# Kernel optimization log

Measured on AMD Instinct MI355X. Metric: run time of the kernel, lower is better.

## Reference

```python
import jax, jax.numpy as jnp
import numpy as np
from jax import lax

DIM = 1024
BATCH = 16
WIDTH = 2048
DECAY = 0.99


def setup_inputs() -> dict:
    key = jax.random.key(0)
    k1, k2, k3, k4 = jax.random.split(key, 4)
    scale = 1.0 / np.sqrt(DIM)
    x = jax.random.normal(k1, (BATCH, WIDTH, DIM), dtype=jnp.float32)
    state = jnp.zeros((BATCH, DIM), dtype=jnp.float32)
    Wv = jax.random.normal(k2, (DIM, DIM), dtype=jnp.float32) * scale
    Wr = jax.random.normal(k3, (DIM, DIM), dtype=jnp.float32) * scale
    Wc = jax.random.normal(k4, (DIM, DIM), dtype=jnp.float32) * scale
    return {"x": x, "state": state, "Wv": Wv, "Wr": Wr, "Wc": Wc}


def reference(x, state, Wv, Wr, Wc):
    # x: [B, W, D], state: [B, D]; fixed-decay RWKV recurrence along width.
    decay = jnp.asarray(DECAY, dtype=x.dtype)
    one_minus = jnp.asarray(1.0, dtype=x.dtype) - decay
    v = jnp.einsum('bwd,de->bwe', x, Wv)                 # value projection
    r = jax.nn.sigmoid(jnp.einsum('bwd,de->bwe', x, Wr))  # receptance

    # scan over width (time) axis: elems shaped [W, B, D]
    def step(s_prev, inp):
        v_t, r_t, x_t = inp
        s_curr = decay * s_prev + one_minus * v_t
        y_t = x_t + r_t * s_curr
        return s_curr, y_t

    elems = (jnp.swapaxes(v, 0, 1), jnp.swapaxes(r, 0, 1), jnp.swapaxes(x, 0, 1))
    new_state, y_t = lax.scan(step, state, elems)
    y = jnp.swapaxes(y_t, 0, 1)                          # [B, W, D]
    y = y + jnp.einsum('bwd,de->bwe', y, Wc)             # minimal channel mix
    return y, new_state
```

## Files before the change

kernel.cpp:

```cpp
#include <hip/hip_runtime.h>
#include <hip/hip_bf16.h>
#include <math.h>


#define DIMK 1024
#define MROWS 32768
#define NCHUNK 16
#define CHUNKL 128
#define DECAY_F 0.99f
#define OM_F 0.01f

typedef __attribute__((ext_vector_type(8))) short short8;
typedef __attribute__((ext_vector_type(4))) float floatx4;

using bf16 = __hip_bfloat16;
using bf162 = __hip_bfloat162;

__global__ void prep_weights(const float* __restrict__ Wv,
                             const float* __restrict__ Wr,
                             const float* __restrict__ Wc,
                             bf16* __restrict__ WT) {
  __shared__ float tile[32][33];
  const int bk = blockIdx.x * 32;
  const int bn = blockIdx.y * 32;
  const float* src;
  int nbase = bn;
  if (bn < 1024)      { src = Wv; }
  else if (bn < 2048) { src = Wr; nbase = bn - 1024; }
  else                { src = Wc; nbase = bn - 2048; }
  const int tx = threadIdx.x;
  const int ty = threadIdx.y;
  #pragma unroll
  for (int i = ty; i < 32; i += 8)
    tile[i][tx] = src[(size_t)(bk + i) * 1024 + nbase + tx];
  __syncthreads();
  #pragma unroll
  for (int i = ty; i < 32; i += 8)
    WT[(size_t)(bn + i) * 1024 + bk + tx] = __float2bfloat16(tile[tx][i]);
}

__global__ __launch_bounds__(256, 2) void gemm_vr(const float* __restrict__ X,
                                                  const bf16* __restrict__ WT,
                                                  bf16* __restrict__ Vout,
                                                  bf16* __restrict__ Rout) {
  __shared__ bf16 As[128][72];
  __shared__ bf16 Bs[128][72];
  const int t = threadIdx.x;
  const int ntile = blockIdx.x;
  const int m0 = blockIdx.y * 128;
  const int lane = t & 63;
  const int wave = t >> 6;
  const int wm = wave >> 1, wn = wave & 1;
  const int ln15 = lane & 15, qd = lane >> 4;

  const bf16* Bsrc = WT + (size_t)(ntile * 128) * 1024;

  floatx4 acc[4][4];
  #pragma unroll
  for (int i = 0; i < 4; ++i)
    #pragma unroll
    for (int j = 0; j < 4; ++j) acc[i][j] = (floatx4){0.f, 0.f, 0.f, 0.f};

  for (int k0 = 0; k0 < 1024; k0 += 64) {
    #pragma unroll
    for (int p = 0; p < 8; ++p) {
      const int f = t + p * 256;
      const int row = f >> 4;
      const int c4 = f & 15;
      const float4 val = *(const float4*)&X[(size_t)(m0 + row) * 1024 + k0 + c4 * 4];
      union { ushort4 u; bf16 h[4]; } pk;
      pk.h[0] = __float2bfloat16(val.x);
      pk.h[1] = __float2bfloat16(val.y);
      pk.h[2] = __float2bfloat16(val.z);
      pk.h[3] = __float2bfloat16(val.w);
      *(ushort4*)&As[row][c4 * 4] = pk.u;
    }
    #pragma unroll
    for (int p = 0; p < 4; ++p) {
      const int o = t + p * 256;
      const int row = o >> 3;
      const int c8 = o & 7;
      const uint4 val = *(const uint4*)&Bsrc[(size_t)row * 1024 + k0 + c8 * 8];
      *(uint4*)&Bs[row][c8 * 8] = val;
    }
    __syncthreads();
    #pragma unroll
    for (int kk = 0; kk < 64; kk += 32) {
      short8 fa[4], fb[4];
      #pragma unroll
      for (int tm = 0; tm < 4; ++tm)
        fa[tm] = *(const short8*)&As[wm * 64 + tm * 16 + ln15][kk + qd * 8];
      #pragma unroll
      for (int tn = 0; tn < 4; ++tn)
        fb[tn] = *(const short8*)&Bs[wn * 64 + tn * 16 + ln15][kk + qd * 8];
      #pragma unroll
      for (int tm = 0; tm < 4; ++tm)
        #pragma unroll
        for (int tn = 0; tn < 4; ++tn)
          acc[tm][tn] = __builtin_amdgcn_mfma_f32_16x16x32_bf16(
              fa[tm], fb[tn], acc[tm][tn], 0, 0, 0);
    }
    __syncthreads();
  }

  const bool isr = (ntile >= 8);
  bf16* outp = isr ? Rout : Vout;
  const int nc0 = (ntile & 7) * 128;
  #pragma unroll
  for (int tm = 0; tm < 4; ++tm) {
    #pragma unroll
    for (int i = 0; i < 4; ++i) {
      const int m_g = m0 + wm * 64 + tm * 16 + qd * 4 + i;
      const size_t rowoff = (size_t)m_g * 1024 + nc0;
      #pragma unroll
      for (int tn = 0; tn < 4; ++tn) {
        float cv = acc[tm][tn][i];
        if (isr) cv = 1.0f / (1.0f + __expf(-cv));
        outp[rowoff + wn * 64 + tn * 16 + ln15] = __float2bfloat16(cv);
      }
    }
  }
}

__global__ void scan_partial(const bf16* __restrict__ V, float* __restrict__ sl) {
  const int idx = blockIdx.x * 256 + threadIdx.x;
  const int d2 = idx & 511;
  const int c = (idx >> 9) & 15;
  const int b = idx >> 13;
  const bf162* V2 = (const bf162*)V;
  const size_t base = (size_t)(b * 2048 + c * 128) * 512 + d2;
  float s0 = 0.f, s1 = 0.f;
  for (int w = 0; w < CHUNKL; ++w) {
    const bf162 v = V2[base + (size_t)w * 512];
    s0 = DECAY_F * s0 + OM_F * __bfloat162float(v.x);
    s1 = DECAY_F * s1 + OM_F * __bfloat162float(v.y);
  }
  const int o = (b * 16 + c) * 1024 + d2 * 2;
  sl[o] = s0;
  sl[o + 1] = s1;
}

__global__ void scan_chunk(const float* __restrict__ state,
                           const float* __restrict__ sl,
                           float* __restrict__ sin_,
                           float* __restrict__ state_out,
                           float decayL) {
  const int idx = blockIdx.x * 256 + threadIdx.x;
  const int d = idx & 1023;
  const int b = idx >> 10;
  float s = state[idx];
  #pragma unroll
  for (int c = 0; c < NCHUNK; ++c) {
    const int o = (b * 16 + c) * 1024 + d;
    sin_[o] = s;
    s = decayL * s + sl[o];
  }
  state_out[idx] = s;
}

__global__ void scan_apply(const float* __restrict__ X,
                           const bf16* __restrict__ R,
                           const float* __restrict__ sin_,
                           bf16* __restrict__ VY) {
  const int idx = blockIdx.x * 256 + threadIdx.x;
  const int d2 = idx & 511;
  const int c = (idx >> 9) & 15;
  const int b = idx >> 13;
  const bf162* R2 = (const bf162*)R;
  bf162* VY2 = (bf162*)VY;
  const float2* X2 = (const float2*)X;
  const size_t base = (size_t)(b * 2048 + c * 128) * 512 + d2;
  const int so = (b * 16 + c) * 1024 + d2 * 2;
  float s0 = sin_[so], s1 = sin_[so + 1];
  for (int w = 0; w < CHUNKL; ++w) {
    const size_t off = base + (size_t)w * 512;
    const bf162 v = VY2[off];
    const bf162 r = R2[off];
    const float2 xx = X2[off];
    s0 = DECAY_F * s0 + OM_F * __bfloat162float(v.x);
    s1 = DECAY_F * s1 + OM_F * __bfloat162float(v.y);
    const float y0 = xx.x + __bfloat162float(r.x) * s0;
    const float y1 = xx.y + __bfloat162float(r.y) * s1;
    bf162 o;
    o.x = __float2bfloat16(y0);
    o.y = __float2bfloat16(y1);
    VY2[off] = o;
  }
}

__global__ __launch_bounds__(256, 2) void gemm_mix(const bf16* __restrict__ Yt,
                                                   const bf16* __restrict__ WcT,
                                                   float* __restrict__ Out) {
  __shared__ bf16 As[128][72];
  __shared__ bf16 Bs[128][72];
  const int t = threadIdx.x;
  const int nc0 = blockIdx.x * 128;
  const int m0 = blockIdx.y * 128;
  const int lane = t & 63;
  const int wave = t >> 6;
  const int wm = wave >> 1, wn = wave & 1;
  const int ln15 = lane & 15, qd = lane >> 4;

  const bf16* Bsrc = WcT + (size_t)nc0 * 1024;

  floatx4 acc[4][4];
  #pragma unroll
  for (int i = 0; i < 4; ++i)
    #pragma unroll
    for (int j = 0; j < 4; ++j) acc[i][j] = (floatx4){0.f, 0.f, 0.f, 0.f};

  for (int k0 = 0; k0 < 1024; k0 += 64) {
    #pragma unroll
    for (int p = 0; p < 4; ++p) {
      const int o = t + p * 256;
      const int row = o >> 3;
      const int c8 = o & 7;
      const uint4 val = *(const uint4*)&Yt[(size_t)(m0 + row) * 1024 + k0 + c8 * 8];
      *(uint4*)&As[row][c8 * 8] = val;
    }
    #pragma unroll
    for (int p = 0; p < 4; ++p) {
      const int o = t + p * 256;
      const int row = o >> 3;
      const int c8 = o & 7;
      const uint4 val = *(const uint4*)&Bsrc[(size_t)row * 1024 + k0 + c8 * 8];
      *(uint4*)&Bs[row][c8 * 8] = val;
    }
    __syncthreads();
    #pragma unroll
    for (int kk = 0; kk < 64; kk += 32) {
      short8 fa[4], fb[4];
      #pragma unroll
      for (int tm = 0; tm < 4; ++tm)
        fa[tm] = *(const short8*)&As[wm * 64 + tm * 16 + ln15][kk + qd * 8];
      #pragma unroll
      for (int tn = 0; tn < 4; ++tn)
        fb[tn] = *(const short8*)&Bs[wn * 64 + tn * 16 + ln15][kk + qd * 8];
      #pragma unroll
      for (int tm = 0; tm < 4; ++tm)
        #pragma unroll
        for (int tn = 0; tn < 4; ++tn)
          acc[tm][tn] = __builtin_amdgcn_mfma_f32_16x16x32_bf16(
              fa[tm], fb[tn], acc[tm][tn], 0, 0, 0);
    }
    __syncthreads();
  }

  #pragma unroll
  for (int tm = 0; tm < 4; ++tm) {
    #pragma unroll
    for (int i = 0; i < 4; ++i) {
      const int m_g = m0 + wm * 64 + tm * 16 + qd * 4 + i;
      const size_t rowoff = (size_t)m_g * 1024 + nc0;
      #pragma unroll
      for (int tn = 0; tn < 4; ++tn) {
        const size_t o = rowoff + wn * 64 + tn * 16 + ln15;
        Out[o] = __bfloat162float(Yt[o]) + acc[tm][tn][i];
      }
    }
  }
}

extern "C" void kernel_launch(void* const* d_in, const int* in_sizes, int n_in,
                              void* d_out, int out_size, void* d_ws, size_t ws_size,
                              hipStream_t stream) {
  const float* x     = (const float*)d_in[0];
  const float* state = (const float*)d_in[1];
  const float* Wv    = (const float*)d_in[2];
  const float* Wr    = (const float*)d_in[3];
  const float* Wc    = (const float*)d_in[4];

  float* y_out = (float*)d_out;
  float* state_out = y_out + (size_t)MROWS * 1024;

  char* ws = (char*)d_ws;
  bf16* WT   = (bf16*)ws;
  bf16* Vbuf = (bf16*)(ws + ((size_t)6 << 20));
  bf16* Rbuf = (bf16*)(ws + ((size_t)70 << 20));
  float* sl  = (float*)(ws + ((size_t)134 << 20));
  float* sin_ = (float*)(ws + ((size_t)135 << 20));
  bf16* WcT = WT + (size_t)2048 * 1024;

  const float decayL = (float)pow(0.99, (double)CHUNKL);

  prep_weights<<<dim3(32, 96), dim3(32, 8), 0, stream>>>(Wv, Wr, Wc, WT);
  gemm_vr<<<dim3(16, 256), 256, 0, stream>>>(x, WT, Vbuf, Rbuf);
  scan_partial<<<512, 256, 0, stream>>>(Vbuf, sl);
  scan_chunk<<<64, 256, 0, stream>>>(state, sl, sin_, state_out, decayL);
  scan_apply<<<512, 256, 0, stream>>>(x, Rbuf, sin_, Vbuf);
  gemm_mix<<<dim3(8, 256), 256, 0, stream>>>(Vbuf, WcT, y_out);
}
```

Before: 578.1 us.

## Pre-convert x to bf16, use global_load_lds async copies, XCD-aware tile mapping

Adds a prep pass that converts x to bf16 once, so both GEMMs and the scan read bf16 and no longer re-convert fp32 in every N-tile. The GEMMs now stage tiles with global_load_lds direct-to-LDS copies, using a K step of 32 with unpadded LDS, and raise the occupancy hint to 3. Block IDs are remapped so adjacent M tiles land on the same XCD for L2 reuse. The risks are LDS bank conflicts from the unpadded layout, more barriers per K, an extra full pass over x, and the scan now adding a bf16-rounded x.

```diff
diff --git a/kernel.cpp b/kernel.cpp
--- a/kernel.cpp
+++ b/kernel.cpp
@@ -3,7 +3,6 @@
 #include <math.h>
 
 
-#define DIMK 1024
 #define MROWS 32768
 #define NCHUNK 16
 #define CHUNKL 128
@@ -15,6 +14,23 @@
 
 using bf16 = __hip_bfloat16;
 using bf162 = __hip_bfloat162;
+
+__device__ __forceinline__ void async_copy16(const bf16* g, bf16* l) {
+  __builtin_amdgcn_global_load_lds(
+      (const __attribute__((address_space(1))) unsigned int*)g,
+      (__attribute__((address_space(3))) unsigned int*)l, 16, 0, 0);
+}
+
+__global__ void prep_x(const float* __restrict__ X, bf16* __restrict__ Xb) {
+  const int idx = blockIdx.x * 256 + threadIdx.x;
+  const float4 v = ((const float4*)X)[idx];
+  union { ushort4 u; bf16 h[4]; } pk;
+  pk.h[0] = __float2bfloat16(v.x);
+  pk.h[1] = __float2bfloat16(v.y);
+  pk.h[2] = __float2bfloat16(v.z);
+  pk.h[3] = __float2bfloat16(v.w);
+  ((ushort4*)Xb)[idx] = pk.u;
+}
 
 __global__ void prep_weights(const float* __restrict__ Wv,
                              const float* __restrict__ Wr,
@@ -39,21 +55,27 @@
     WT[(size_t)(bn + i) * 1024 + bk + tx] = __float2bfloat16(tile[tx][i]);
 }
 
-__global__ __launch_bounds__(256, 2) void gemm_vr(const float* __restrict__ X,
+__global__ __launch_bounds__(256, 3) void gemm_vr(const bf16* __restrict__ Xb,
                                                   const bf16* __restrict__ WT,
                                                   bf16* __restrict__ Vout,
                                                   bf16* __restrict__ Rout) {
-  __shared__ bf16 As[128][72];
-  __shared__ bf16 Bs[128][72];
+  __shared__ bf16 As[128][32];
+  __shared__ bf16 Bs[128][32];
   const int t = threadIdx.x;
-  const int ntile = blockIdx.x;
-  const int m0 = blockIdx.y * 128;
-  const int lane = t & 63;
-  const int wave = t >> 6;
+  const int id = blockIdx.x;
+  const int grp = id >> 3, xcd = id & 7;
+  const int mt = ((grp >> 4) << 3) | xcd;
+  const int nt = grp & 15;
+  const int m0 = mt * 128;
+  const int lane = t & 63, wave = t >> 6;
   const int wm = wave >> 1, wn = wave & 1;
   const int ln15 = lane & 15, qd = lane >> 4;
 
-  const bf16* Bsrc = WT + (size_t)(ntile * 128) * 1024;
+  const bf16* Asrc = Xb + (size_t)m0 * 1024;
+  const bf16* Bsrc = WT + (size_t)(nt * 128) * 1024;
+
+  const int srow = lane >> 2;
+  const int skb  = (lane & 3) * 8;
 
   floatx4 acc[4][4];
   #pragma unroll
@@ -61,51 +83,34 @@
     #pragma unroll
     for (int j = 0; j < 4; ++j) acc[i][j] = (floatx4){0.f, 0.f, 0.f, 0.f};
 
-  for (int k0 = 0; k0 < 1024; k0 += 64) {
-    #pragma unroll
-    for (int p = 0; p < 8; ++p) {
-      const int f = t + p * 256;
-      const int row = f >> 4;
-      const int c4 = f & 15;
-      const float4 val = *(const float4*)&X[(size_t)(m0 + row) * 1024 + k0 + c4 * 4];
-      union { ushort4 u; bf16 h[4]; } pk;
-      pk.h[0] = __float2bfloat16(val.x);
-      pk.h[1] = __float2bfloat16(val.y);
-      pk.h[2] = __float2bfloat16(val.z);
-      pk.h[3] = __float2bfloat16(val.w);
-      *(ushort4*)&As[row][c4 * 4] = pk.u;
-    }
-    #pragma unroll
-    for (int p = 0; p < 4; ++p) {
-      const int o = t + p * 256;
-      const int row = o >> 3;
-      const int c8 = o & 7;
-      const uint4 val = *(const uint4*)&Bsrc[(size_t)row * 1024 + k0 + c8 * 8];
-      *(uint4*)&Bs[row][c8 * 8] = val;
-    }
-    __syncthreads();
-    #pragma unroll
-    for (int kk = 0; kk < 64; kk += 32) {
-      short8 fa[4], fb[4];
-      #pragma unroll
-      for (int tm = 0; tm < 4; ++tm)
-        fa[tm] = *(const short8*)&As[wm * 64 + tm * 16 + ln15][kk + qd * 8];
+  for (int k0 = 0; k0 < 1024; k0 += 32) {
+    #pragma unroll
+    for (int s = 0; s < 2; ++s) {
+      const int seg = wave * 2 + s;
+      const size_t roff = (size_t)(seg * 16 + srow) * 1024 + k0 + skb;
+      async_copy16(&Asrc[roff], &As[seg * 16][0]);
+      async_copy16(&Bsrc[roff], &Bs[seg * 16][0]);
+    }
+    __syncthreads();
+    short8 fa[4], fb[4];
+    #pragma unroll
+    for (int tm = 0; tm < 4; ++tm)
+      fa[tm] = *(const short8*)&As[wm * 64 + tm * 16 + ln15][qd * 8];
+    #pragma unroll
+    for (int tn = 0; tn < 4; ++tn)
+      fb[tn] = *(const short8*)&Bs[wn * 64 + tn * 16 + ln15][qd * 8];
+    #pragma unroll
+    for (int tm = 0; tm < 4; ++tm)
       #pragma unroll
       for (int tn = 0; tn < 4; ++tn)
-        fb[tn] = *(const short8*)&Bs[wn * 64 + tn * 16 + ln15][kk + qd * 8];
-      #pragma unroll
-      for (int tm = 0; tm < 4; ++tm)
-        #pragma unroll
-        for (int tn = 0; tn < 4; ++tn)
-          acc[tm][tn] = __builtin_amdgcn_mfma_f32_16x16x32_bf16(
-              fa[tm], fb[tn], acc[tm][tn], 0, 0, 0);
-    }
-    __syncthreads();
-  }
-
-  const bool isr = (ntile >= 8);
+        acc[tm][tn] = __builtin_amdgcn_mfma_f32_16x16x32_bf16(
+            fa[tm], fb[tn], acc[tm][tn], 0, 0, 0);
+    __syncthreads();
+  }
+
+  const bool isr = (nt >= 8);
   bf16* outp = isr ? Rout : Vout;
-  const int nc0 = (ntile & 7) * 128;
+  const int nc0 = (nt & 7) * 128;
   #pragma unroll
   for (int tm = 0; tm < 4; ++tm) {
     #pragma unroll
@@ -158,7 +163,7 @@
   state_out[idx] = s;
 }
 
-__global__ void scan_apply(const float* __restrict__ X,
+__global__ void scan_apply(const bf16* __restrict__ Xb,
                            const bf16* __restrict__ R,
                            const float* __restrict__ sin_,
                            bf16* __restrict__ VY) {
@@ -167,8 +172,8 @@
   const int c = (idx >> 9) & 15;
   const int b = idx >> 13;
   const bf162* R2 = (const bf162*)R;
+  const bf162* X2 = (const bf162*)Xb;
   bf162* VY2 = (bf162*)VY;
-  const float2* X2 = (const float2*)X;
   const size_t base = (size_t)(b * 2048 + c * 128) * 512 + d2;
   const int so = (b * 16 + c) * 1024 + d2 * 2;
   float s0 = sin_[so], s1 = sin_[so + 1];
@@ -176,11 +181,11 @@
     const size_t off = base + (size_t)w * 512;
     const bf162 v = VY2[off];
     const bf162 r = R2[off];
-    const float2 xx = X2[off];
+    const bf162 xx = X2[off];
     s0 = DECAY_F * s0 + OM_F * __bfloat162float(v.x);
     s1 = DECAY_F * s1 + OM_F * __bfloat162float(v.y);
-    const float y0 = xx.x + __bfloat162float(r.x) * s0;
-    const float y1 = xx.y + __bfloat162float(r.y) * s1;
+    const float y0 = __bfloat162float(xx.x) + __bfloat162float(r.x) * s0;
+    const float y1 = __bfloat162float(xx.y) + __bfloat162float(r.y) * s1;
     bf162 o;
     o.x = __float2bfloat16(y0);
     o.y = __float2bfloat16(y1);
@@ -188,61 +193,56 @@
   }
 }
 
-__global__ __launch_bounds__(256, 2) void gemm_mix(const bf16* __restrict__ Yt,
+__global__ __launch_bounds__(256, 3) void gemm_mix(const bf16* __restrict__ Yt,
                                                    const bf16* __restrict__ WcT,
                                                    float* __restrict__ Out) {
-  __shared__ bf16 As[128][72];
-  __shared__ bf16 Bs[128][72];
+  __shared__ bf16 As[128][32];
+  __shared__ bf16 Bs[128][32];
   const int t = threadIdx.x;
-  const int nc0 = blockIdx.x * 128;
-  const int m0 = blockIdx.y * 128;
-  const int lane = t & 63;
-  const int wave = t >> 6;
+  const int id = blockIdx.x;
+  const int grp = id >> 3, xcd = id & 7;
+  const int mt = ((grp >> 3) << 3) | xcd;
+  const int nt = grp & 7;
+  const int m0 = mt * 128;
+  const int nc0 = nt * 128;
+  const int lane = t & 63, wave = t >> 6;
   const int wm = wave >> 1, wn = wave & 1;
   const int ln15 = lane & 15, qd = lane >> 4;
 
+  const bf16* Asrc = Yt + (size_t)m0 * 1024;
   const bf16* Bsrc = WcT + (size_t)nc0 * 1024;
 
+  const int srow = lane >> 2;
+  const int skb  = (lane & 3) * 8;
+
   floatx4 acc[4][4];
   #pragma unroll
   for (int i = 0; i < 4; ++i)
     #pragma unroll
     for (int j = 0; j < 4; ++j) acc[i][j] = (floatx4){0.f, 0.f, 0.f, 0.f};
 
-  for (int k0 = 0; k0 < 1024; k0 += 64) {
-    #pragma unroll
-    for (int p = 0; p < 4; ++p) {
-      const int o = t + p * 256;
-      const int row = o >> 3;
-      const int c8 = o & 7;
-      const uint4 val = *(const uint4*)&Yt[(size_t)(m0 + row) * 1024 + k0 + c8 * 8];
-      *(uint4*)&As[row][c8 * 8] = val;
-    }
-    #pragma unroll
-    for (int p = 0; p < 4; ++p) {
-      const int o = t + p * 256;
-      const int row = o >> 3;
-      const int c8 = o & 7;
-      const uint4 val = *(const uint4*)&Bsrc[(size_t)row * 1024 + k0 + c8 * 8];
-      *(uint4*)&Bs[row][c8 * 8] = val;
-    }
-    __syncthreads();
-    #pragma unroll
-    for (int kk = 0; kk < 64; kk += 32) {
-      short8 fa[4], fb[4];
-      #pragma unroll
-      for (int tm = 0; tm < 4; ++tm)
-        fa[tm] = *(const short8*)&As[wm * 64 + tm * 16 + ln15][kk + qd * 8];
+  for (int k0 = 0; k0 < 1024; k0 += 32) {
+    #pragma unroll
+    for (int s = 0; s < 2; ++s) {
+      const int seg = wave * 2 + s;
+      const size_t roff = (size_t)(seg * 16 + srow) * 1024 + k0 + skb;
+      async_copy16(&Asrc[roff], &As[seg * 16][0]);
+      async_copy16(&Bsrc[roff], &Bs[seg * 16][0]);
+    }
+    __syncthreads();
+    short8 fa[4], fb[4];
+    #pragma unroll
+    for (int tm = 0; tm < 4; ++tm)
+      fa[tm] = *(const short8*)&As[wm * 64 + tm * 16 + ln15][qd * 8];
+    #pragma unroll
+    for (int tn = 0; tn < 4; ++tn)
+      fb[tn] = *(const short8*)&Bs[wn * 64 + tn * 16 + ln15][qd * 8];
+    #pragma unroll
+    for (int tm = 0; tm < 4; ++tm)
       #pragma unroll
       for (int tn = 0; tn < 4; ++tn)
-        fb[tn] = *(const short8*)&Bs[wn * 64 + tn * 16 + ln15][kk + qd * 8];
-      #pragma unroll
-      for (int tm = 0; tm < 4; ++tm)
-        #pragma unroll
-        for (int tn = 0; tn < 4; ++tn)
-          acc[tm][tn] = __builtin_amdgcn_mfma_f32_16x16x32_bf16(
-              fa[tm], fb[tn], acc[tm][tn], 0, 0, 0);
-    }
+        acc[tm][tn] = __builtin_amdgcn_mfma_f32_16x16x32_bf16(
+            fa[tm], fb[tn], acc[tm][tn], 0, 0, 0);
     __syncthreads();
   }
 
@@ -275,18 +275,20 @@
 
   char* ws = (char*)d_ws;
   bf16* WT   = (bf16*)ws;
-  bf16* Vbuf = (bf16*)(ws + ((size_t)6 << 20));
-  bf16* Rbuf = (bf16*)(ws + ((size_t)70 << 20));
-  float* sl  = (float*)(ws + ((size_t)134 << 20));
-  float* sin_ = (float*)(ws + ((size_t)135 << 20));
+  bf16* Xb   = (bf16*)(ws + ((size_t)6 << 20));
+  bf16* Vbuf = (bf16*)(ws + ((size_t)70 << 20));
+  bf16* Rbuf = (bf16*)(ws + ((size_t)134 << 20));
+  float* sl  = (float*)(ws + ((size_t)198 << 20));
+  float* sin_ = (float*)(ws + ((size_t)199 << 20));
   bf16* WcT = WT + (size_t)2048 * 1024;
 
   const float decayL = (float)pow(0.99, (double)CHUNKL);
 
+  prep_x<<<32768, 256, 0, stream>>>(x, Xb);
   prep_weights<<<dim3(32, 96), dim3(32, 8), 0, stream>>>(Wv, Wr, Wc, WT);
-  gemm_vr<<<dim3(16, 256), 256, 0, stream>>>(x, WT, Vbuf, Rbuf);
+  gemm_vr<<<4096, 256, 0, stream>>>(Xb, WT, Vbuf, Rbuf);
   scan_partial<<<512, 256, 0, stream>>>(Vbuf, sl);
   scan_chunk<<<64, 256, 0, stream>>>(state, sl, sin_, state_out, decayL);
-  scan_apply<<<512, 256, 0, stream>>>(x, Rbuf, sin_, Vbuf);
-  gemm_mix<<<dim3(8, 256), 256, 0, stream>>>(Vbuf, WcT, y_out);
-}
+  scan_apply<<<512, 256, 0, stream>>>(Xb, Rbuf, sin_, Vbuf);
+  gemm_mix<<<2048, 256, 0, stream>>>(Vbuf, WcT, y_out);
+}
```

Measured after the change: 529.4 us. 1.09x faster.
